# Performance work log

Hardware: AMD Instinct MI355X
Metric: run time of the kernel (lower is better)

## Reference

```python
import jax, jax.numpy as jnp
import numpy as np

OBS_LEN = 20
PRED_LEN = 30
NUM_MODES = 6
DATA_DIM = 2
DROPOUT_P = 0.25
NEG_SLOPE = 0.01
H_DIM = 256
B = 8192


def setup_inputs() -> dict:
    key = jax.random.key(0)
    ks = jax.random.split(key, 20)
    s = 0.05
    inp = {
        "traj_abs": jax.random.normal(ks[0], (OBS_LEN, B, DATA_DIM), jnp.float32),
        "traj_rel": jax.random.normal(ks[1], (OBS_LEN, B, DATA_DIM), jnp.float32),
        "state_h": jax.random.normal(ks[2], (1, B, H_DIM), jnp.float32),
        "c0": jax.random.normal(ks[3], (NUM_MODES, B, H_DIM), jnp.float32),
        # spatial embedding Linear(40, 40)
        "W_se": jax.random.normal(ks[4], (OBS_LEN * 2, OBS_LEN * 2), jnp.float32) * s,
        "b_se": jax.random.normal(ks[5], (OBS_LEN * 2,), jnp.float32) * s,
        # LSTM weights: input 40 -> hidden 256, gates order i,f,g,o
        "W_ih": jax.random.normal(ks[6], (4 * H_DIM, OBS_LEN * 2), jnp.float32) * s,
        "W_hh": jax.random.normal(ks[7], (4 * H_DIM, H_DIM), jnp.float32) * s,
        "b_ih": jax.random.normal(ks[8], (4 * H_DIM,), jnp.float32) * s,
        "b_hh": jax.random.normal(ks[9], (4 * H_DIM,), jnp.float32) * s,
        # per-mode prediction heads Linear(256, 2)
        "W_pred": jax.random.normal(ks[10], (NUM_MODES, DATA_DIM, H_DIM), jnp.float32) * s,
        "b_pred": jax.random.normal(ks[11], (NUM_MODES, DATA_DIM), jnp.float32) * s,
        # confidence PredictionNet (norm=False), latent = PRED_LEN*DATA_DIM = 60
        "pn_w1": jax.random.normal(ks[12], (PRED_LEN * DATA_DIM, PRED_LEN * DATA_DIM), jnp.float32) * s,
        "pn_b1": jax.random.normal(ks[13], (PRED_LEN * DATA_DIM,), jnp.float32) * s,
        "pn_w2": jax.random.normal(ks[14], (PRED_LEN * DATA_DIM, PRED_LEN * DATA_DIM), jnp.float32) * s,
        "pn_b2": jax.random.normal(ks[15], (PRED_LEN * DATA_DIM,), jnp.float32) * s,
        "pn_wfc": jax.random.normal(ks[16], (1, PRED_LEN * DATA_DIM), jnp.float32) * s,
        "pn_bfc": jax.random.normal(ks[17], (1,), jnp.float32) * s,
    }
    return inp


def _decode(traj_rel, state_h, c0, W_se, b_se, W_ih, W_hh, b_ih, b_hh,
            W_pred, b_pred, pn_w1, pn_b1, pn_w2, pn_b2, pn_wfc, pn_bfc):
    batch = traj_rel.shape[1]
    h0 = state_h[0]  # (B, H)
    keep = 1.0 - DROPOUT_P
    # one dropout key per (mode, step); deterministic stand-in for torch dropout
    keys = jax.random.split(jax.random.key(42), NUM_MODES * PRED_LEN).reshape(NUM_MODES, PRED_LEN)

    def one_mode(Wp, bp, c0m, keys_m):
        def step(carry, key):
            h, c, buf = carry  # buf: (OBS_LEN, B, 2) rolling window of rel displacements
            x = buf.transpose(1, 0, 2).reshape(batch, -1) @ W_se.T + b_se  # (B, 40)
            x = jnp.where(x > 0, x, NEG_SLOPE * x)  # leaky_relu
            mask = jax.random.bernoulli(key, keep, x.shape)
            x = jnp.where(mask, x / keep, 0.0)  # dropout (training=True)
            gates = x @ W_ih.T + b_ih + h @ W_hh.T + b_hh  # (B, 4H)
            i, f, g, o = jnp.split(gates, 4, axis=-1)
            c = jax.nn.sigmoid(f) * c + jax.nn.sigmoid(i) * jnp.tanh(g)
            h = jax.nn.sigmoid(o) * jnp.tanh(c)
            rel = h @ Wp.T + bp  # (B, 2)
            buf = jnp.roll(buf, -1, axis=0).at[-1].set(rel)
            return (h, c, buf), rel

        _, rels = jax.lax.scan(step, (h0, c0m, traj_rel), keys_m)
        return rels  # (PRED_LEN, B, 2)

    rels = jax.vmap(one_mode)(W_pred, b_pred, c0, keys)  # (M, T, B, 2)
    pred = rels.transpose(2, 0, 1, 3)  # (B, M, T, 2)

    # confidence PredictionNet (norm=False)
    x = pred.reshape(batch, NUM_MODES, PRED_LEN * DATA_DIM)
    y = jax.nn.relu(x @ pn_w1.T + pn_b1)
    y = jax.nn.relu(y @ pn_w2.T + pn_b2 + x)
    conf = (y @ pn_wfc.T + pn_bfc).reshape(batch, NUM_MODES)
    conf = jax.nn.softmax(conf, axis=1)
    return pred, conf


def reference(traj_abs, traj_rel, state_h, c0, W_se, b_se, W_ih, W_hh, b_ih, b_hh,
              W_pred, b_pred, pn_w1, pn_b1, pn_w2, pn_b2, pn_wfc, pn_bfc):
    # traj_abs unused in the 'Latent' branch (only its shape is read)
    return _decode(traj_rel, state_h, c0, W_se, b_se, W_ih, W_hh, b_ih, b_hh,
                   W_pred, b_pred, pn_w1, pn_b1, pn_w2, pn_b2, pn_wfc, pn_bfc)
```

## Files before the change

kernel.cpp:

```cpp
#include <hip/hip_runtime.h>
#include <cstdint>

#define JAX_PARTITIONABLE 1

#define OBS_LEN 20
#define PRED_LEN 30
#define NUM_MODES 6
#define BATCH 8192
#define H 256
#define MB (NUM_MODES * BATCH)
#define KPAD 320

typedef __attribute__((ext_vector_type(8))) short bf16x8;
typedef __attribute__((ext_vector_type(4))) float f32x4;

__host__ __device__ inline void tf2x32(uint32_t k0, uint32_t k1, uint32_t c0, uint32_t c1,
                                       uint32_t& o0, uint32_t& o1) {
  uint32_t ks0 = k0, ks1 = k1, ks2 = k0 ^ k1 ^ 0x1BD11BDAu;
  uint32_t x0 = c0 + ks0, x1 = c1 + ks1;
#define TF_R(x, r) (((x) << (r)) | ((x) >> (32 - (r))))
#define TF_RND(r)  { x0 += x1; x1 = TF_R(x1, r); x1 ^= x0; }
  TF_RND(13) TF_RND(15) TF_RND(26) TF_RND(6)   x0 += ks1; x1 += ks2 + 1u;
  TF_RND(17) TF_RND(29) TF_RND(16) TF_RND(24)  x0 += ks2; x1 += ks0 + 2u;
  TF_RND(13) TF_RND(15) TF_RND(26) TF_RND(6)   x0 += ks0; x1 += ks1 + 3u;
  TF_RND(17) TF_RND(29) TF_RND(16) TF_RND(24)  x0 += ks1; x1 += ks2 + 4u;
  TF_RND(13) TF_RND(15) TF_RND(26) TF_RND(6)   x0 += ks2; x1 += ks0 + 5u;
  o0 = x0; o1 = x1;
#undef TF_RND
#undef TF_R
}

__device__ inline void step_key(int m, int t, uint32_t& k0, uint32_t& k1) {
#if JAX_PARTITIONABLE
  tf2x32(0u, 42u, 0u, (uint32_t)(m * PRED_LEN + t), k0, k1);
#else
  int i = m * PRED_LEN + t;
  int n0 = 2 * i, n1 = 2 * i + 1;
  uint32_t a0, a1;
  if (n0 < 180) { tf2x32(0u, 42u, (uint32_t)n0, (uint32_t)(n0 + 180), a0, a1); k0 = a0; }
  else          { tf2x32(0u, 42u, (uint32_t)(n0 - 180), (uint32_t)n0, a0, a1); k0 = a1; }
  if (n1 < 180) { tf2x32(0u, 42u, (uint32_t)n1, (uint32_t)(n1 + 180), a0, a1); k1 = a0; }
  else          { tf2x32(0u, 42u, (uint32_t)(n1 - 180), (uint32_t)n1, a0, a1); k1 = a1; }
#endif
}

__device__ inline uint32_t mask_bits(uint32_t k0, uint32_t k1, uint32_t n) {
#if JAX_PARTITIONABLE
  uint32_t o0, o1;
  tf2x32(k0, k1, 0u, n, o0, o1);
  return o0 ^ o1;
#else
  const uint32_t HALF = (uint32_t)(BATCH * 40 / 2);
  uint32_t o0, o1;
  if (n < HALF) { tf2x32(k0, k1, n, n + HALF, o0, o1); return o0; }
  else          { tf2x32(k0, k1, n - HALF, n, o0, o1); return o1; }
#endif
}

__device__ __forceinline__ float sigf(float x) { return 1.0f / (1.0f + __expf(-x)); }
__device__ __forceinline__ float tanhfast(float x) {
  float e = __expf(-2.0f * fabsf(x));
  float t = (1.0f - e) / (1.0f + e);
  return x >= 0.f ? t : -t;
}
__device__ __forceinline__ ushort f2bf(float f) {
  uint32_t u = __float_as_uint(f);
  uint32_t r = (u + 0x7fffu + ((u >> 16) & 1u)) >> 16;
  return (ushort)r;
}
__device__ __forceinline__ float bf2f(uint32_t u) { return __uint_as_float(u << 16); }

__global__ __launch_bounds__(256) void k_prep(const float* __restrict__ Wih, const float* __restrict__ Whh,
                                              const float* __restrict__ bih, const float* __restrict__ bhh,
                                              ushort* __restrict__ WTb, float* __restrict__ bias) {
  int idx = blockIdx.x * 256 + threadIdx.x;
  if (idx < 1024 * KPAD) {
    int np = idx / KPAD, k = idx - np * KPAD;
    int cg = np >> 7, r = np & 127;
    int nt = r >> 4, col = r & 15;
    int N = (nt & 3) * 256 + cg * 32 + (nt >> 2) * 16 + col;
    float v = (k < 40) ? Wih[N * 40 + k] : (k < 296 ? Whh[N * 256 + (k - 40)] : 0.f);
    WTb[idx] = f2bf(v);
  }
  if (idx < 1024) bias[idx] = bih[idx] + bhh[idx];
}

__global__ __launch_bounds__(256) void k_init(const float* __restrict__ state_h, const float* __restrict__ c0,
                                              float* __restrict__ cst, ushort* __restrict__ Ab0,
                                              ushort* __restrict__ Ab1) {
  int idx = blockIdx.x * 256 + threadIdx.x;
  if (idx < MB * 64) {
    int row = idx >> 6;
    int j4 = (idx & 63) << 2;
    float4 cv = *(const float4*)(c0 + (size_t)idx * 4);
    *(float4*)(cst + (size_t)idx * 4) = cv;
    int b = row & (BATCH - 1);
    float4 hv = *(const float4*)(state_h + (size_t)b * H + j4);
    ushort4 hb = {f2bf(hv.x), f2bf(hv.y), f2bf(hv.z), f2bf(hv.w)};
    *(ushort4*)(Ab0 + (size_t)row * KPAD + 40 + j4) = hb;
  }
  if (idx < MB * 6) {
    int row = idx / 6, p4 = (idx - row * 6) << 2;
    ushort4 z = {0, 0, 0, 0};
    *(ushort4*)(Ab0 + (size_t)row * KPAD + 296 + p4) = z;
    *(ushort4*)(Ab1 + (size_t)row * KPAD + 296 + p4) = z;
  }
}

__global__ __launch_bounds__(256) void k_embed(const float* __restrict__ traj_rel, const float* __restrict__ rels,
                                               const float* __restrict__ Wse, const float* __restrict__ bse,
                                               ushort* __restrict__ Ax, int t) {
  __shared__ float sW[1600];
  __shared__ float sb[40];
  int tid = threadIdx.x;
  for (int i = tid; i < 1600; i += 256) sW[i] = Wse[i];
  if (tid < 40) sb[tid] = bse[tid];
  __syncthreads();
  int gid = blockIdx.x * 256 + tid;
  int b = gid & (BATCH - 1);
  int m = gid >> 13;
  float win[40];
#pragma unroll
  for (int kk = 0; kk < OBS_LEN; kk++) {
    int st = t + kk;
    const float* p = (st < OBS_LEN)
        ? (traj_rel + (((size_t)st * BATCH + b) << 1))
        : (rels + (((size_t)(m * PRED_LEN + (st - OBS_LEN)) * BATCH + b) << 1));
    float2 w = *(const float2*)p;
    win[kk * 2] = w.x; win[kk * 2 + 1] = w.y;
  }
  uint32_t k0, k1;
  step_key(m, t, k0, k1);
  uint32_t nb = (uint32_t)(b * 40);
  ushort* orow = Ax + (size_t)gid * KPAD;
#pragma unroll
  for (int jo = 0; jo < 5; jo++) {
    uint32_t pk[4];
#pragma unroll
    for (int jp = 0; jp < 4; jp++) {
      ushort lo = 0, hi = 0;
#pragma unroll
      for (int ji = 0; ji < 2; ji++) {
        int j = jo * 8 + jp * 2 + ji;
        float a = sb[j];
#pragma unroll
        for (int p = 0; p < 40; p += 4) {
          float4 w = *(const float4*)&sW[j * 40 + p];
          a = fmaf(win[p + 3], w.w, fmaf(win[p + 2], w.z, fmaf(win[p + 1], w.y, fmaf(win[p], w.x, a))));
        }
        a = a > 0.f ? a : 0.01f * a;
        uint32_t bits = mask_bits(k0, k1, nb + (uint32_t)j);
        float u = __uint_as_float((bits >> 9) | 0x3f800000u) - 1.0f;
        ushort r = (u < 0.75f) ? f2bf(a * 1.3333333730697632f) : (ushort)0;
        if (ji == 0) lo = r; else hi = r;
      }
      pk[jp] = (uint32_t)lo | ((uint32_t)hi << 16);
    }
    uint4 v = {pk[0], pk[1], pk[2], pk[3]};
    *(uint4*)(orow + jo * 8) = v;
  }
}

__global__ __launch_bounds__(256) void k_gates(const ushort* __restrict__ Ain, const ushort* __restrict__ WTb,
                                               const float* __restrict__ bias, float* __restrict__ cst,
                                               ushort* __restrict__ Anext) {
  __shared__ __align__(16) ushort lA[2][128][40];
  __shared__ __align__(16) ushort lB[2][128][40];
  int tid = threadIdx.x;
  int w = tid >> 6, lane = tid & 63;
  int row0 = blockIdx.x * 128;
  int cg = blockIdx.y;
  int sr = tid >> 1, sh = (tid & 1) << 4;
  const ushort* gA = Ain + (size_t)(row0 + sr) * KPAD + sh;
  const ushort* gB = WTb + (size_t)(cg * 128 + sr) * KPAD + sh;

  f32x4 zero = {0.f, 0.f, 0.f, 0.f};
  f32x4 acc[2][8];
#pragma unroll
  for (int i = 0; i < 2; i++)
#pragma unroll
    for (int j = 0; j < 8; j++) acc[i][j] = zero;

  uint4 ra0 = *(const uint4*)gA;
  uint4 ra1 = *(const uint4*)(gA + 8);
  uint4 rb0 = *(const uint4*)gB;
  uint4 rb1 = *(const uint4*)(gB + 8);
  *(uint4*)&lA[0][sr][sh] = ra0;
  *(uint4*)&lA[0][sr][sh + 8] = ra1;
  *(uint4*)&lB[0][sr][sh] = rb0;
  *(uint4*)&lB[0][sr][sh + 8] = rb1;
  __syncthreads();

  int fm = lane & 15, fq = lane >> 4;
  for (int kt = 0; kt < 10; kt++) {
    int cur = kt & 1;
    if (kt < 9) {
      ra0 = *(const uint4*)(gA + (kt + 1) * 32);
      ra1 = *(const uint4*)(gA + (kt + 1) * 32 + 8);
      rb0 = *(const uint4*)(gB + (kt + 1) * 32);
      rb1 = *(const uint4*)(gB + (kt + 1) * 32 + 8);
    }
    bf16x8 af[2], bfr[8];
#pragma unroll
    for (int rt = 0; rt < 2; rt++) af[rt] = *(const bf16x8*)&lA[cur][w * 32 + rt * 16 + fm][fq * 8];
#pragma unroll
    for (int nt = 0; nt < 8; nt++) bfr[nt] = *(const bf16x8*)&lB[cur][nt * 16 + fm][fq * 8];
#pragma unroll
    for (int rt = 0; rt < 2; rt++)
#pragma unroll
      for (int nt = 0; nt < 8; nt++)
        acc[rt][nt] = __builtin_amdgcn_mfma_f32_16x16x32_bf16(af[rt], bfr[nt], acc[rt][nt], 0, 0, 0);
    if (kt < 9) {
      *(uint4*)&lA[cur ^ 1][sr][sh] = ra0;
      *(uint4*)&lA[cur ^ 1][sr][sh + 8] = ra1;
      *(uint4*)&lB[cur ^ 1][sr][sh] = rb0;
      *(uint4*)&lB[cur ^ 1][sr][sh + 8] = rb1;
      __syncthreads();
    }
  }

#pragma unroll
  for (int jg = 0; jg < 2; jg++) {
    int jh = cg * 32 + jg * 16 + fm;
    float bi = bias[jh], bfg = bias[256 + jh], bg = bias[512 + jh], bo = bias[768 + jh];
#pragma unroll
    for (int rt = 0; rt < 2; rt++) {
#pragma unroll
      for (int reg = 0; reg < 4; reg++) {
        int row = row0 + w * 32 + rt * 16 + fq * 4 + reg;
        float gi = acc[rt][jg * 4 + 0][reg] + bi;
        float gf = acc[rt][jg * 4 + 1][reg] + bfg;
        float gg = acc[rt][jg * 4 + 2][reg] + bg;
        float go = acc[rt][jg * 4 + 3][reg] + bo;
        size_t ci = (size_t)row * H + jh;
        float cv = cst[ci];
        float c2 = sigf(gf) * cv + sigf(gi) * tanhfast(gg);
        cst[ci] = c2;
        float hn = sigf(go) * tanhfast(c2);
        Anext[(size_t)row * KPAD + 40 + jh] = f2bf(hn);
      }
    }
  }
}

__global__ __launch_bounds__(256) void k_predembed(const ushort* __restrict__ hsrc, const float* __restrict__ Wp,
                                                   const float* __restrict__ bp, float* __restrict__ rels,
                                                   const float* __restrict__ traj_rel,
                                                   const float* __restrict__ Wse, const float* __restrict__ bse,
                                                   ushort* __restrict__ Ax, int t) {
  __shared__ float sW[1600];
  __shared__ float sb[40];
  int tid = threadIdx.x;
  for (int i = tid; i < 1600; i += 256) sW[i] = Wse[i];
  if (tid < 40) sb[tid] = bse[tid];
  __syncthreads();
  int wv = tid >> 6, lane = tid & 63;
  int grp = lane >> 3, lg = lane & 7;
  int row = blockIdx.x * 32 + wv * 8 + grp;
  int m = row / BATCH, b = row & (BATCH - 1);

  const ushort* hr = hsrc + (size_t)row * KPAD + 40 + lg * 32;
  const float* w0 = Wp + m * 512 + lg * 32;
  const float* w1 = w0 + 256;
  float s0 = 0.f, s1 = 0.f;
#pragma unroll
  for (int q = 0; q < 4; q++) {
    uint4 hv = *(const uint4*)(hr + q * 8);
    float h0 = bf2f(hv.x & 0xffffu), h1 = bf2f(hv.x >> 16);
    float h2 = bf2f(hv.y & 0xffffu), h3 = bf2f(hv.y >> 16);
    float h4 = bf2f(hv.z & 0xffffu), h5 = bf2f(hv.z >> 16);
    float h6 = bf2f(hv.w & 0xffffu), h7 = bf2f(hv.w >> 16);
    float4 wa0 = *(const float4*)(w0 + q * 8);
    float4 wa1 = *(const float4*)(w0 + q * 8 + 4);
    float4 wb0 = *(const float4*)(w1 + q * 8);
    float4 wb1 = *(const float4*)(w1 + q * 8 + 4);
    s0 += h0 * wa0.x + h1 * wa0.y + h2 * wa0.z + h3 * wa0.w
        + h4 * wa1.x + h5 * wa1.y + h6 * wa1.z + h7 * wa1.w;
    s1 += h0 * wb0.x + h1 * wb0.y + h2 * wb0.z + h3 * wb0.w
        + h4 * wb1.x + h5 * wb1.y + h6 * wb1.z + h7 * wb1.w;
  }
#pragma unroll
  for (int off = 1; off < 8; off <<= 1) {
    s0 += __shfl_xor(s0, off, 64);
    s1 += __shfl_xor(s1, off, 64);
  }
  float relx = s0 + bp[m * 2];
  float rely = s1 + bp[m * 2 + 1];
  if (lg == 0) {
    *(float2*)(rels + ((size_t)(m * PRED_LEN + t) * BATCH + b) * 2) = make_float2(relx, rely);
  }

  int te = t + 1;
  float win[40];
#pragma unroll
  for (int kk = 0; kk < OBS_LEN; kk++) {
    int st = te + kk;
    float2 w2;
    if (st < OBS_LEN) {
      w2 = *(const float2*)(traj_rel + (((size_t)st * BATCH + b) << 1));
    } else if (st - OBS_LEN == t) {
      w2 = make_float2(relx, rely);
    } else {
      w2 = *(const float2*)(rels + (((size_t)(m * PRED_LEN + (st - OBS_LEN)) * BATCH + b) << 1));
    }
    win[kk * 2] = w2.x; win[kk * 2 + 1] = w2.y;
  }
  uint32_t k0, k1;
  step_key(m, te, k0, k1);
  uint32_t nb = (uint32_t)(b * 40);
  ushort* orow = Ax + (size_t)row * KPAD;
#pragma unroll
  for (int u = 0; u < 5; u++) {
    int j = lg * 5 + u;
    float a = sb[j];
#pragma unroll
    for (int p = 0; p < 40; p += 4) {
      float4 w = *(const float4*)&sW[j * 40 + p];
      a = fmaf(win[p + 3], w.w, fmaf(win[p + 2], w.z, fmaf(win[p + 1], w.y, fmaf(win[p], w.x, a))));
    }
    a = a > 0.f ? a : 0.01f * a;
    uint32_t bits = mask_bits(k0, k1, nb + (uint32_t)j);
    float uu = __uint_as_float((bits >> 9) | 0x3f800000u) - 1.0f;
    orow[j] = (uu < 0.75f) ? f2bf(a * 1.3333333730697632f) : (ushort)0;
  }
}

__global__ __launch_bounds__(256) void k_transconf(const float* __restrict__ rels,
                                                   const float* __restrict__ W1, const float* __restrict__ b1,
                                                   const float* __restrict__ W2, const float* __restrict__ b2,
                                                   const float* __restrict__ wfc, const float* __restrict__ bfc,
                                                   float* __restrict__ out) {
  __shared__ float tile[32][361];
  __shared__ float sW1[3600];
  __shared__ float sW2[3600];
  __shared__ float sb1[60], sb2[60], swfc[60];
  __shared__ float sy1[192][61];
  __shared__ float slg[32][6];
  int tid = threadIdx.x;
  for (int i = tid; i < 3600; i += 256) { sW1[i] = W1[i]; sW2[i] = W2[i]; }
  if (tid < 60) { sb1[tid] = b1[tid]; sb2[tid] = b2[tid]; swfc[tid] = wfc[tid]; }
  int b0 = blockIdx.x * 32;
  for (int i = tid; i < 11520; i += 256) {
    int bl = i & 31, c = i >> 5;
    int mm = c / 60, r = c % 60;
    tile[bl][c] = rels[((size_t)((mm * PRED_LEN + (r >> 1)) * BATCH) + (b0 + bl)) * 2 + (r & 1)];
  }
  __syncthreads();
  for (int i = tid; i < 11520; i += 256) {
    int bl = i / 360, c = i % 360;
    out[(size_t)(b0 + bl) * 360 + c] = tile[bl][c];
  }
  if (tid < 192) {
    int bl = tid / 6, mm = tid - bl * 6;
    int xb = mm * 60;
    for (int q = 0; q < 60; q++) {
      float acl = sb1[q];
#pragma unroll
      for (int p = 0; p < 60; p++) acl = fmaf(tile[bl][xb + p], sW1[q * 60 + p], acl);
      sy1[tid][q] = fmaxf(acl, 0.f);
    }
    float logit = bfc[0];
    for (int q = 0; q < 60; q++) {
      float acl = sb2[q] + tile[bl][xb + q];
#pragma unroll
      for (int p = 0; p < 60; p++) acl = fmaf(sy1[tid][p], sW2[q * 60 + p], acl);
      logit = fmaf(fmaxf(acl, 0.f), swfc[q], logit);
    }
    slg[bl][mm] = logit;
  }
  __syncthreads();
  if (tid < 32) {
    float mx = slg[tid][0];
#pragma unroll
    for (int m = 1; m < 6; m++) mx = fmaxf(mx, slg[tid][m]);
    float e[6], s = 0.f;
#pragma unroll
    for (int m = 0; m < 6; m++) { e[m] = __expf(slg[tid][m] - mx); s += e[m]; }
    float inv = 1.0f / s;
    size_t base = (size_t)BATCH * 360 + (size_t)(b0 + tid) * 6;
#pragma unroll
    for (int m = 0; m < 6; m++) out[base + m] = e[m] * inv;
  }
}

extern "C" void kernel_launch(void* const* d_in, const int* in_sizes, int n_in,
                              void* d_out, int out_size, void* d_ws, size_t ws_size,
                              hipStream_t stream) {
  const float* traj_rel = (const float*)d_in[1];
  const float* state_h  = (const float*)d_in[2];
  const float* c0       = (const float*)d_in[3];
  const float* Wse      = (const float*)d_in[4];
  const float* bse      = (const float*)d_in[5];
  const float* Wih      = (const float*)d_in[6];
  const float* Whh      = (const float*)d_in[7];
  const float* bih      = (const float*)d_in[8];
  const float* bhh      = (const float*)d_in[9];
  const float* Wp       = (const float*)d_in[10];
  const float* bp       = (const float*)d_in[11];
  const float* W1       = (const float*)d_in[12];
  const float* b1       = (const float*)d_in[13];
  const float* W2       = (const float*)d_in[14];
  const float* b2       = (const float*)d_in[15];
  const float* wfc      = (const float*)d_in[16];
  const float* bfc      = (const float*)d_in[17];
  float* out = (float*)d_out;

  float* cst  = (float*)d_ws;
  float* rels = cst + (size_t)MB * H;
  float* bias = rels + (size_t)NUM_MODES * PRED_LEN * BATCH * 2;
  ushort* WTb = (ushort*)(bias + 1024);
  ushort* Ab0 = WTb + (size_t)1024 * KPAD;
  ushort* Ab1 = Ab0 + (size_t)MB * KPAD;

  k_prep<<<1280, 256, 0, stream>>>(Wih, Whh, bih, bhh, WTb, bias);
  k_init<<<12288, 256, 0, stream>>>(state_h, c0, cst, Ab0, Ab1);
  k_embed<<<192, 256, 0, stream>>>(traj_rel, rels, Wse, bse, Ab0, 0);
  for (int t = 0; t < PRED_LEN; t++) {
    ushort* Acur  = (t & 1) ? Ab1 : Ab0;
    ushort* Anext = (t & 1) ? Ab0 : Ab1;
    k_gates<<<dim3(384, 8), 256, 0, stream>>>(Acur, WTb, bias, cst, Anext);
    k_predembed<<<1536, 256, 0, stream>>>(Anext, Wp, bp, rels, traj_rel, Wse, bse, Anext, t);
  }
  k_transconf<<<256, 256, 0, stream>>>(rels, W1, b1, W2, b2, wfc, bfc, out);
}
```

Measured before the change: 3.351 ms.

## Stage gate GEMM tiles via direct global-to-LDS loads with XOR swizzle

Replaces the register-staged double buffer in the LSTM gate GEMM kernel with buffer loads that write straight into LDS (global_load_lds, 16 bytes per lane). The padded LDS rows are dropped in favour of an XOR swizzle that avoids bank conflicts, and the launch bounds request three blocks per CU. This removes the VGPR round trip and the explicit LDS stores and cuts LDS footprint to raise occupancy. It relies on correct synchronisation of the async LDS writes and on the swizzle matching between writer and reader.

```diff
diff --git a/kernel.cpp b/kernel.cpp
--- a/kernel.cpp
+++ b/kernel.cpp
@@ -161,18 +161,37 @@
   }
 }
 
-__global__ __launch_bounds__(256) void k_gates(const ushort* __restrict__ Ain, const ushort* __restrict__ WTb,
-                                               const float* __restrict__ bias, float* __restrict__ cst,
-                                               ushort* __restrict__ Anext) {
-  __shared__ __align__(16) ushort lA[2][128][40];
-  __shared__ __align__(16) ushort lB[2][128][40];
+__global__ __launch_bounds__(256, 3) void k_gates(const ushort* __restrict__ Ain, const ushort* __restrict__ WTb,
+                                                  const float* __restrict__ bias, float* __restrict__ cst,
+                                                  ushort* __restrict__ Anext) {
+  __shared__ __align__(16) ushort lA[2][128][32];
+  __shared__ __align__(16) ushort lB[2][128][32];
   int tid = threadIdx.x;
   int w = tid >> 6, lane = tid & 63;
   int row0 = blockIdx.x * 128;
   int cg = blockIdx.y;
-  int sr = tid >> 1, sh = (tid & 1) << 4;
-  const ushort* gA = Ain + (size_t)(row0 + sr) * KPAD + sh;
-  const ushort* gB = WTb + (size_t)(cg * 128 + sr) * KPAD + sh;
+  int fm = lane & 15, fq = lane >> 4;
+  int srow = lane >> 2;
+  int sg = (lane & 3) ^ ((lane >> 3) & 3);
+  const ushort* gA0 = Ain + (size_t)(row0 + w * 32 + srow) * KPAD + sg * 8;
+  const ushort* gA1 = Ain + (size_t)(row0 + w * 32 + 16 + srow) * KPAD + sg * 8;
+  const ushort* gB0 = WTb + (size_t)(cg * 128 + w * 32 + srow) * KPAD + sg * 8;
+  const ushort* gB1 = WTb + (size_t)(cg * 128 + w * 32 + 16 + srow) * KPAD + sg * 8;
+
+#define STAGE(buf, kt) {                                                                      \
+    __builtin_amdgcn_global_load_lds(                                                         \
+        (const __attribute__((address_space(1))) uint32_t*)(gA0 + (kt) * 32),                 \
+        (__attribute__((address_space(3))) uint32_t*)&lA[buf][w * 32][0], 16, 0, 0);          \
+    __builtin_amdgcn_global_load_lds(                                                         \
+        (const __attribute__((address_space(1))) uint32_t*)(gA1 + (kt) * 32),                 \
+        (__attribute__((address_space(3))) uint32_t*)&lA[buf][w * 32 + 16][0], 16, 0, 0);     \
+    __builtin_amdgcn_global_load_lds(                                                         \
+        (const __attribute__((address_space(1))) uint32_t*)(gB0 + (kt) * 32),                 \
+        (__attribute__((address_space(3))) uint32_t*)&lB[buf][w * 32][0], 16, 0, 0);          \
+    __builtin_amdgcn_global_load_lds(                                                         \
+        (const __attribute__((address_space(1))) uint32_t*)(gB1 + (kt) * 32),                 \
+        (__attribute__((address_space(3))) uint32_t*)&lB[buf][w * 32 + 16][0], 16, 0, 0);     \
+  }
 
   f32x4 zero = {0.f, 0.f, 0.f, 0.f};
   f32x4 acc[2][8];
@@ -181,43 +200,26 @@
 #pragma unroll
     for (int j = 0; j < 8; j++) acc[i][j] = zero;
 
-  uint4 ra0 = *(const uint4*)gA;
-  uint4 ra1 = *(const uint4*)(gA + 8);
-  uint4 rb0 = *(const uint4*)gB;
-  uint4 rb1 = *(const uint4*)(gB + 8);
-  *(uint4*)&lA[0][sr][sh] = ra0;
-  *(uint4*)&lA[0][sr][sh + 8] = ra1;
-  *(uint4*)&lB[0][sr][sh] = rb0;
-  *(uint4*)&lB[0][sr][sh + 8] = rb1;
+  STAGE(0, 0);
   __syncthreads();
 
-  int fm = lane & 15, fq = lane >> 4;
+  int soff = (fq ^ ((fm >> 1) & 3)) * 8;
   for (int kt = 0; kt < 10; kt++) {
     int cur = kt & 1;
-    if (kt < 9) {
-      ra0 = *(const uint4*)(gA + (kt + 1) * 32);
-      ra1 = *(const uint4*)(gA + (kt + 1) * 32 + 8);
-      rb0 = *(const uint4*)(gB + (kt + 1) * 32);
-      rb1 = *(const uint4*)(gB + (kt + 1) * 32 + 8);
-    }
+    if (kt < 9) STAGE(cur ^ 1, kt + 1);
     bf16x8 af[2], bfr[8];
 #pragma unroll
-    for (int rt = 0; rt < 2; rt++) af[rt] = *(const bf16x8*)&lA[cur][w * 32 + rt * 16 + fm][fq * 8];
-#pragma unroll
-    for (int nt = 0; nt < 8; nt++) bfr[nt] = *(const bf16x8*)&lB[cur][nt * 16 + fm][fq * 8];
+    for (int rt = 0; rt < 2; rt++) af[rt] = *(const bf16x8*)&lA[cur][w * 32 + rt * 16 + fm][soff];
+#pragma unroll
+    for (int nt = 0; nt < 8; nt++) bfr[nt] = *(const bf16x8*)&lB[cur][nt * 16 + fm][soff];
 #pragma unroll
     for (int rt = 0; rt < 2; rt++)
 #pragma unroll
       for (int nt = 0; nt < 8; nt++)
         acc[rt][nt] = __builtin_amdgcn_mfma_f32_16x16x32_bf16(af[rt], bfr[nt], acc[rt][nt], 0, 0, 0);
-    if (kt < 9) {
-      *(uint4*)&lA[cur ^ 1][sr][sh] = ra0;
-      *(uint4*)&lA[cur ^ 1][sr][sh + 8] = ra1;
-      *(uint4*)&lB[cur ^ 1][sr][sh] = rb0;
-      *(uint4*)&lB[cur ^ 1][sr][sh + 8] = rb1;
-      __syncthreads();
-    }
-  }
+    if (kt < 9) __syncthreads();
+  }
+#undef STAGE
 
 #pragma unroll
   for (int jg = 0; jg < 2; jg++) {
```

After: 3.333 ms. About the same (-0.5%).
